# Kernel optimization log

Measured on AMD Instinct MI355X. Metric: run time of the kernel, lower is better.

Reference implementation:

```python
import jax, jax.numpy as jnp
import numpy as np

B, C, H, W = 4, 64, 64, 64  # in_dim hardcoded to 64 by the module's views


def _conv1x1(x, w, b):
    # x: [B,C,H,W], w: [O,C], b: [O]
    return jnp.einsum('bchw,oc->bohw', x, w) + b[None, :, None, None]


def _branch(x, wq, bq, wk, bk, wv, bv):
    b_, c_, h_, w_ = x.shape
    n = h_ * w_
    q = _conv1x1(x, wq, bq).reshape(b_, c_, n)
    k = _conv1x1(x, wk, bk).reshape(b_, c_, n)
    v = _conv1x1(x, wv, bv).reshape(b_, c_, n)
    # scores[b,i,j] = sum_c q[b,c,i] * k[b,c,j]  (no scale factor, as in source)
    s = jax.nn.softmax(jnp.einsum('bci,bcj->bij', q, k), axis=-1)  # [B,N,N]
    # out[b,c,j] = sum_i v[b,c,i] * s[b,i,j]
    return jnp.einsum('bci,bij->bcj', v, s).reshape(b_, c_, h_, w_)


def setup_inputs() -> dict:
    key = jax.random.key(0)
    ks = jax.random.split(key, 17)
    sc = 1.0 / np.sqrt(C)
    d = {'x': jax.random.normal(ks[0], (B, C, H, W), jnp.float32)}
    names = ['qh', 'kh', 'vh', 'ql', 'kl', 'vl']
    for i, nm in enumerate(names):
        d['W_' + nm] = jax.random.normal(ks[1 + 2 * i], (C, C), jnp.float32) * sc
        d['b_' + nm] = jax.random.normal(ks[2 + 2 * i], (C,), jnp.float32) * 0.01
    d['g1'] = jax.random.normal(ks[13], (1,), jnp.float32) * 0.5
    d['g2'] = jax.random.normal(ks[14], (1,), jnp.float32) * 0.5
    d['W_f'] = jax.random.normal(ks[15], (C, 2 * C), jnp.float32) * (1.0 / np.sqrt(2 * C))
    d['b_f'] = jax.random.normal(ks[16], (C,), jnp.float32) * 0.01
    return d


def reference(x, W_qh, b_qh, W_kh, b_kh, W_vh, b_vh, W_ql, b_ql, W_kl, b_kl, W_vl, b_vl, g1, g2, W_f, b_f):
    xh1 = g1[0] * _branch(x, W_qh, b_qh, W_kh, b_kh, W_vh, b_vh)
    xl1 = g2[0] * _branch(x, W_ql, b_ql, W_kl, b_kl, W_vl, b_vl)
    cat = jnp.concatenate([xh1, xl1], axis=1)  # [B,2C,H,W]
    return _conv1x1(cat, W_f, b_f)
```

## Files before the change

kernel.cpp:

```cpp
#include <hip/hip_runtime.h>

#define NN 4096
#define CD 64

typedef __attribute__((ext_vector_type(8))) short bf16x8;
typedef __attribute__((ext_vector_type(4))) float f32x4;

__device__ unsigned short g_Qh[2][4][NN][CD];
__device__ unsigned short g_Ql[2][4][NN][CD];
__device__ unsigned short g_Kh[2][4][NN][CD];
__device__ unsigned short g_Kl[2][4][NN][CD];
__device__ float          g_Vf[2][4][CD][NN];
__device__ unsigned short g_Vh[2][4][CD][NN];
__device__ unsigned short g_Vl[2][4][CD][NN];
__device__ float          g_Op[4][2][4][CD][NN];
__device__ float          g_Zp[4][2][4][NN];

__device__ inline f32x4 mfma16(bf16x8 a, bf16x8 b, f32x4 c) {
  return __builtin_amdgcn_mfma_f32_16x16x32_bf16(a, b, c, 0, 0, 0);
}

__device__ inline void split_bf(float x, unsigned short& h, unsigned short& l) {
  unsigned u = __builtin_bit_cast(unsigned, x);
  h = (unsigned short)(u >> 16);
  float hf = __builtin_bit_cast(float, u & 0xffff0000u);
  unsigned v = __builtin_bit_cast(unsigned, x - hf);
  v += 0x7fffu + ((v >> 16) & 1u);
  l = (unsigned short)(v >> 16);
}

__device__ inline void lds_barrier() {
  asm volatile("s_waitcnt lgkmcnt(0)\n\ts_barrier" ::: "memory");
}

struct ProjArgs {
  const float* x;
  const float* W[6];
  const float* bias[6];
};

__global__ __launch_bounds__(256) void proj_kernel(ProjArgs a) {
  __shared__ float Wt[64][68];
  __shared__ float bs[64];
  const int tid = threadIdx.x;
  const int m = blockIdx.z;
  const float* __restrict__ W = a.W[m];
#pragma unroll
  for (int k = 0; k < 16; ++k) {
    int t = k * 256 + tid;
    Wt[t & 63][t >> 6] = W[t];
  }
  if (tid < 64) bs[tid] = a.bias[m][tid];
  __syncthreads();

  const int b = blockIdx.y;
  const int n = (blockIdx.x << 6) + (tid & 63);
  const int og = tid >> 6;
  const float* __restrict__ xp = a.x + ((size_t)b * CD) * NN + n;

  float acc[16];
#pragma unroll
  for (int k = 0; k < 16; ++k) acc[k] = bs[og * 16 + k];

#pragma unroll 4
  for (int c = 0; c < 64; ++c) {
    float xv = xp[(size_t)c * NN];
    float w[16];
    *(float4*)&w[0]  = *(const float4*)&Wt[c][og * 16 + 0];
    *(float4*)&w[4]  = *(const float4*)&Wt[c][og * 16 + 4];
    *(float4*)&w[8]  = *(const float4*)&Wt[c][og * 16 + 8];
    *(float4*)&w[12] = *(const float4*)&Wt[c][og * 16 + 12];
#pragma unroll
    for (int k = 0; k < 16; ++k) acc[k] += w[k] * xv;
  }

  const int br = m / 3, kind = m % 3;
  if (kind == 2) {
    float* dst = &g_Vf[br][b][0][0] + n;
#pragma unroll
    for (int k = 0; k < 16; ++k) dst[(size_t)(og * 16 + k) * NN] = acc[k];
  } else {
    unsigned short hi[16], lo[16];
#pragma unroll
    for (int k = 0; k < 16; ++k) split_bf(acc[k], hi[k], lo[k]);
    unsigned short* dh = (kind == 0) ? &g_Qh[br][b][n][og * 16] : &g_Kh[br][b][n][og * 16];
    unsigned short* dl = (kind == 0) ? &g_Ql[br][b][n][og * 16] : &g_Kl[br][b][n][og * 16];
    *(uint4*)dh       = *(const uint4*)&hi[0];
    *(uint4*)(dh + 8) = *(const uint4*)&hi[8];
    *(uint4*)dl       = *(const uint4*)&lo[0];
    *(uint4*)(dl + 8) = *(const uint4*)&lo[8];
  }
}

__global__ __launch_bounds__(256) void pass1_kernel() {
  __shared__ float zbuf[2][64];

  const int tid = threadIdx.x;
  const int bid = blockIdx.x;
  const int img = bid & 7;
  const int br = img >> 2, b = img & 3;
  const int js = (bid >> 3) & 3;
  const int i0 = (bid >> 5) << 6;

  const int lane = tid & 63, w = tid >> 6;
  const int wi = w >> 1, wj = w & 1;
  const int lm = lane & 15, q = lane >> 4;

  const unsigned short* __restrict__ QhB = &g_Qh[br][b][0][0];
  const unsigned short* __restrict__ QlB = &g_Ql[br][b][0][0];
  const unsigned short* __restrict__ KhB = &g_Kh[br][b][0][0];
  const unsigned short* __restrict__ KlB = &g_Kl[br][b][0][0];

  bf16x8 qa[2][2][2];
#pragma unroll
  for (int it = 0; it < 2; ++it)
#pragma unroll
    for (int cs = 0; cs < 2; ++cs) {
      size_t off = (size_t)(i0 + wi * 32 + it * 16 + lm) * 64 + cs * 32 + q * 8;
      qa[it][cs][0] = *(const bf16x8*)(QhB + off);
      qa[it][cs][1] = *(const bf16x8*)(QlB + off);
    }

  float zacc[2][4];
#pragma unroll
  for (int it = 0; it < 2; ++it)
#pragma unroll
    for (int r = 0; r < 4; ++r) zacc[it][r] = 0.f;

  const int jwave = wj * 32 + lm;
  for (int tt = 0; tt < 16; ++tt) {
    const int jb = ((js << 4) + tt) << 6;

    bf16x8 kb[2][2][2];
#pragma unroll
    for (int jt = 0; jt < 2; ++jt) {
      size_t rowo = (size_t)(jb + jwave + jt * 16) * 64 + q * 8;
#pragma unroll
      for (int cs = 0; cs < 2; ++cs) {
        kb[jt][cs][0] = *(const bf16x8*)(KhB + rowo + cs * 32);
        kb[jt][cs][1] = *(const bf16x8*)(KlB + rowo + cs * 32);
      }
    }

    const f32x4 zf = {0.f, 0.f, 0.f, 0.f};
#pragma unroll
    for (int it = 0; it < 2; ++it)
#pragma unroll
      for (int jt = 0; jt < 2; ++jt) {
        f32x4 s = mfma16(qa[it][0][0], kb[jt][0][0], zf);
        s = mfma16(qa[it][1][0], kb[jt][1][0], s);
        s = mfma16(qa[it][0][0], kb[jt][0][1], s);
        s = mfma16(qa[it][1][0], kb[jt][1][1], s);
        s = mfma16(qa[it][0][1], kb[jt][0][0], s);
        s = mfma16(qa[it][1][1], kb[jt][1][0], s);
        zacc[it][0] += __expf(s[0]);
        zacc[it][1] += __expf(s[1]);
        zacc[it][2] += __expf(s[2]);
        zacc[it][3] += __expf(s[3]);
      }
  }

#pragma unroll
  for (int mm = 1; mm < 16; mm <<= 1)
#pragma unroll
    for (int it = 0; it < 2; ++it)
#pragma unroll
      for (int r = 0; r < 4; ++r) zacc[it][r] += __shfl_xor(zacc[it][r], mm, 64);

  if (lm == 0) {
#pragma unroll
    for (int it = 0; it < 2; ++it)
#pragma unroll
      for (int r = 0; r < 4; ++r)
        zbuf[wj][wi * 32 + it * 16 + q * 4 + r] = zacc[it][r];
  }
  __syncthreads();
  if (tid < 64) g_Zp[js][br][b][i0 + tid] = zbuf[0][tid] + zbuf[1][tid];
}

__global__ __launch_bounds__(256) void scalev_kernel(const float* __restrict__ g1,
                                                     const float* __restrict__ g2) {
  int idx = blockIdx.x * 256 + threadIdx.x;
  int i4 = idx & 1023;
  int c  = (idx >> 10) & 63;
  int b  = (idx >> 16) & 3;
  int br = idx >> 18;
  float g = br ? g2[0] : g1[0];
  float4 z0 = *(const float4*)&g_Zp[0][br][b][i4 * 4];
  float4 z1 = *(const float4*)&g_Zp[1][br][b][i4 * 4];
  float4 z2 = *(const float4*)&g_Zp[2][br][b][i4 * 4];
  float4 z3 = *(const float4*)&g_Zp[3][br][b][i4 * 4];
  float4 z = {z0.x + z1.x + z2.x + z3.x, z0.y + z1.y + z2.y + z3.y,
              z0.z + z1.z + z2.z + z3.z, z0.w + z1.w + z2.w + z3.w};
  float4 v = *(const float4*)&g_Vf[br][b][c][i4 * 4];
  float vv[4] = {v.x * g / z.x, v.y * g / z.y, v.z * g / z.z, v.w * g / z.w};
  unsigned short h[4], l[4];
#pragma unroll
  for (int r = 0; r < 4; ++r) split_bf(vv[r], h[r], l[r]);
  uint2 uh, ul;
  uh.x = (unsigned)h[0] | ((unsigned)h[1] << 16);
  uh.y = (unsigned)h[2] | ((unsigned)h[3] << 16);
  ul.x = (unsigned)l[0] | ((unsigned)l[1] << 16);
  ul.y = (unsigned)l[2] | ((unsigned)l[3] << 16);
  *(uint2*)&g_Vh[br][b][c][i4 * 4] = uh;
  *(uint2*)&g_Vl[br][b][c][i4 * 4] = ul;
}

__global__ __launch_bounds__(256, 2) void pass2_kernel() {
  __shared__ unsigned short pt_h[64 * 64];
  __shared__ unsigned short pt_l[64 * 64];

  const int tid = threadIdx.x;
  const int bid = blockIdx.x;
  const int img = bid & 7;
  const int br = img >> 2, b = img & 3;
  const int is = (bid >> 3) & 3;
  const int j0 = (bid >> 5) << 6;

  const int lane = tid & 63, w = tid >> 6;
  const int wi = w >> 1, wj = w & 1;
  const int lm = lane & 15, q = lane >> 4;

  const unsigned short* __restrict__ QhB = &g_Qh[br][b][0][0];
  const unsigned short* __restrict__ QlB = &g_Ql[br][b][0][0];
  const unsigned short* __restrict__ KhB = &g_Kh[br][b][0][0];
  const unsigned short* __restrict__ KlB = &g_Kl[br][b][0][0];
  const unsigned short* __restrict__ VhB = &g_Vh[br][b][0][0];
  const unsigned short* __restrict__ VlB = &g_Vl[br][b][0][0];

  bf16x8 kb[2][2][2];
#pragma unroll
  for (int jt = 0; jt < 2; ++jt)
#pragma unroll
    for (int cs = 0; cs < 2; ++cs) {
      size_t off = (size_t)(j0 + wj * 32 + jt * 16 + lm) * 64 + cs * 32 + q * 8;
      kb[jt][cs][0] = *(const bf16x8*)(KhB + off);
      kb[jt][cs][1] = *(const bf16x8*)(KlB + off);
    }

  bf16x8 qa[2][2][2];
  bf16x8 va[2][2][2];
  auto loadQ = [&](int ib) {
#pragma unroll
    for (int it = 0; it < 2; ++it)
#pragma unroll
      for (int cs = 0; cs < 2; ++cs) {
        size_t off = (size_t)(ib + wi * 32 + it * 16 + lm) * 64 + cs * 32 + q * 8;
        qa[it][cs][0] = *(const bf16x8*)(QhB + off);
        qa[it][cs][1] = *(const bf16x8*)(QlB + off);
      }
  };
  auto loadV = [&](int ib) {
#pragma unroll
    for (int ct = 0; ct < 2; ++ct)
#pragma unroll
      for (int ks = 0; ks < 2; ++ks) {
        size_t off = (size_t)(wi * 32 + ct * 16 + lm) * NN + ib + ks * 32 + q * 8;
        va[ct][ks][0] = *(const bf16x8*)(VhB + off);
        va[ct][ks][1] = *(const bf16x8*)(VlB + off);
      }
  };
  const int ibase = is << 10;
  loadQ(ibase);
  loadV(ibase);

  f32x4 oacc[2][2];
#pragma unroll
  for (int ct = 0; ct < 2; ++ct)
#pragma unroll
    for (int jt = 0; jt < 2; ++jt) oacc[ct][jt] = (f32x4){0.f, 0.f, 0.f, 0.f};

  for (int tt = 0; tt < 16; ++tt) {
    const int inext = ibase + ((tt + 1) << 6);
    const f32x4 zf = {0.f, 0.f, 0.f, 0.f};
    f32x4 sacc[2][2];
#pragma unroll
    for (int it = 0; it < 2; ++it)
#pragma unroll
      for (int jt = 0; jt < 2; ++jt) {
        f32x4 s = mfma16(qa[it][0][0], kb[jt][0][0], zf);
        s = mfma16(qa[it][1][0], kb[jt][1][0], s);
        s = mfma16(qa[it][0][0], kb[jt][0][1], s);
        s = mfma16(qa[it][1][0], kb[jt][1][1], s);
        s = mfma16(qa[it][0][1], kb[jt][0][0], s);
        s = mfma16(qa[it][1][1], kb[jt][1][0], s);
        sacc[it][jt] = s;
      }
    if (tt < 15) loadQ(inext);

    uint2 wh[2][2], wl[2][2];
#pragma unroll
    for (int it = 0; it < 2; ++it)
#pragma unroll
      for (int jt = 0; jt < 2; ++jt) {
        unsigned short h[4], l[4];
#pragma unroll
        for (int r = 0; r < 4; ++r) {
          float e = __expf(sacc[it][jt][r]);
          split_bf(e, h[r], l[r]);
        }
        wh[it][jt].x = (unsigned)h[0] | ((unsigned)h[1] << 16);
        wh[it][jt].y = (unsigned)h[2] | ((unsigned)h[3] << 16);
        wl[it][jt].x = (unsigned)l[0] | ((unsigned)l[1] << 16);
        wl[it][jt].y = (unsigned)l[2] | ((unsigned)l[3] << 16);
      }

    lds_barrier();
#pragma unroll
    for (int it = 0; it < 2; ++it)
#pragma unroll
      for (int jt = 0; jt < 2; ++jt) {
        int row = wj * 32 + jt * 16 + lm;
        int byte = row * 128 + (((wi * 64) + it * 32 + q * 8) ^ ((row & 7) << 4));
        *(uint2*)((char*)pt_h + byte) = wh[it][jt];
        *(uint2*)((char*)pt_l + byte) = wl[it][jt];
      }
    lds_barrier();

    bf16x8 pb[2][2][2];
#pragma unroll
    for (int jt = 0; jt < 2; ++jt) {
      int row = wj * 32 + jt * 16 + lm;
      int rb = row * 128, sw = (row & 7) << 4;
#pragma unroll
      for (int ks = 0; ks < 2; ++ks) {
        int byte = rb + ((ks * 64 + q * 16) ^ sw);
        pb[jt][ks][0] = *(const bf16x8*)((const char*)pt_h + byte);
        pb[jt][ks][1] = *(const bf16x8*)((const char*)pt_l + byte);
      }
    }
#pragma unroll
    for (int ct = 0; ct < 2; ++ct)
#pragma unroll
      for (int jt = 0; jt < 2; ++jt) {
        f32x4 o = oacc[ct][jt];
        o = mfma16(va[ct][0][0], pb[jt][0][0], o);
        o = mfma16(va[ct][1][0], pb[jt][1][0], o);
        o = mfma16(va[ct][0][0], pb[jt][0][1], o);
        o = mfma16(va[ct][1][0], pb[jt][1][1], o);
        o = mfma16(va[ct][0][1], pb[jt][0][0], o);
        o = mfma16(va[ct][1][1], pb[jt][1][0], o);
        oacc[ct][jt] = o;
      }
    if (tt < 15) loadV(inext);
  }

  float* __restrict__ Ob = &g_Op[is][br][b][0][0];
#pragma unroll
  for (int ct = 0; ct < 2; ++ct)
#pragma unroll
    for (int jt = 0; jt < 2; ++jt)
#pragma unroll
      for (int r = 0; r < 4; ++r)
        Ob[(size_t)(wi * 32 + ct * 16 + q * 4 + r) * NN + j0 + wj * 32 + jt * 16 + lm] =
            oacc[ct][jt][r];
}

__global__ __launch_bounds__(256) void final_kernel(const float* __restrict__ Wf,
                                                    const float* __restrict__ bf,
                                                    float* __restrict__ out) {
  __shared__ float Wt[128][68];
  __shared__ float bs[64];
  const int tid = threadIdx.x;
#pragma unroll
  for (int k = 0; k < 32; ++k) {
    int t = k * 256 + tid;
    Wt[t & 127][t >> 7] = Wf[t];
  }
  if (tid < 64) bs[tid] = bf[tid];
  __syncthreads();

  const int b = blockIdx.y;
  const int n = (blockIdx.x << 6) + (tid & 63);
  const int og = tid >> 6;
  const size_t PS = (size_t)2 * 4 * CD * NN;

  float acc[16];
#pragma unroll
  for (int k = 0; k < 16; ++k) acc[k] = bs[og * 16 + k];

#pragma unroll
  for (int br = 0; br < 2; ++br) {
    const float* __restrict__ Ob = &g_Op[0][br][b][0][0];
#pragma unroll 4
    for (int c = 0; c < 64; ++c) {
      const float* p = Ob + (size_t)c * NN + n;
      float xv = p[0] + p[PS] + p[2 * PS] + p[3 * PS];
      float wv[16];
      *(float4*)&wv[0]  = *(const float4*)&Wt[br * 64 + c][og * 16 + 0];
      *(float4*)&wv[4]  = *(const float4*)&Wt[br * 64 + c][og * 16 + 4];
      *(float4*)&wv[8]  = *(const float4*)&Wt[br * 64 + c][og * 16 + 8];
      *(float4*)&wv[12] = *(const float4*)&Wt[br * 64 + c][og * 16 + 12];
#pragma unroll
      for (int k = 0; k < 16; ++k) acc[k] += wv[k] * xv;
    }
  }

  float* op = out + ((size_t)b * CD) * NN + n;
#pragma unroll
  for (int k = 0; k < 16; ++k) op[(size_t)(og * 16 + k) * NN] = acc[k];
}

extern "C" void kernel_launch(void* const* d_in, const int* in_sizes, int n_in,
                              void* d_out, int out_size, void* d_ws, size_t ws_size,
                              hipStream_t stream) {
  (void)in_sizes; (void)n_in; (void)d_ws; (void)ws_size; (void)out_size;

  ProjArgs pa;
  pa.x = (const float*)d_in[0];
  for (int m = 0; m < 6; ++m) {
    pa.W[m]    = (const float*)d_in[1 + 2 * m];
    pa.bias[m] = (const float*)d_in[2 + 2 * m];
  }
  const float* g1 = (const float*)d_in[13];
  const float* g2 = (const float*)d_in[14];
  const float* Wf = (const float*)d_in[15];
  const float* bf = (const float*)d_in[16];
  float* out = (float*)d_out;

  proj_kernel<<<dim3(64, 4, 6), 256, 0, stream>>>(pa);
  pass1_kernel<<<dim3(2048), 256, 0, stream>>>();
  scalev_kernel<<<dim3(2048), 256, 0, stream>>>(g1, g2);
  pass2_kernel<<<dim3(2048), 256, 0, stream>>>();
  final_kernel<<<dim3(64, 4), 256, 0, stream>>>(Wf, bf, out);
}
```

Before: 487.5 us.

## Drop low bf16 parts of P and V, restructure pass2 per-wave columns

The second attention pass now uses a single bf16 for the probabilities and the scaled V instead of hi/lo split pairs, which cuts the MFMA count in the PV product by a factor of three and halves V traffic. pass2 is reorganised so each wave owns 16 output columns and loops over all 64 i-tiles, which removes the cross-wave LDS barriers and the 4-way partial-output reduction in final_kernel. pass1 gains K register double-buffering, and both passes raise wave priority with s_setprio around the MFMA blocks. The risks are lower accuracy from single-bf16 P and V, and fewer, longer blocks (512), which may reduce parallelism.

```diff
diff --git a/kernel.cpp b/kernel.cpp
--- a/kernel.cpp
+++ b/kernel.cpp
@@ -11,9 +11,8 @@
 __device__ unsigned short g_Kh[2][4][NN][CD];
 __device__ unsigned short g_Kl[2][4][NN][CD];
 __device__ float          g_Vf[2][4][CD][NN];
-__device__ unsigned short g_Vh[2][4][CD][NN];
-__device__ unsigned short g_Vl[2][4][CD][NN];
-__device__ float          g_Op[4][2][4][CD][NN];
+__device__ unsigned short g_Vb[2][4][CD][NN];
+__device__ float          g_O [2][4][CD][NN];
 __device__ float          g_Zp[4][2][4][NN];
 
 __device__ inline f32x4 mfma16(bf16x8 a, bf16x8 b, f32x4 c) {
@@ -29,8 +28,12 @@
   l = (unsigned short)(v >> 16);
 }
 
-__device__ inline void lds_barrier() {
-  asm volatile("s_waitcnt lgkmcnt(0)\n\ts_barrier" ::: "memory");
+__device__ inline unsigned rne2(float a, float b) {
+  unsigned ua = __builtin_bit_cast(unsigned, a);
+  unsigned ub = __builtin_bit_cast(unsigned, b);
+  ua += 0x7fffu + ((ua >> 16) & 1u);
+  ub += 0x7fffu + ((ub >> 16) & 1u);
+  return (ua >> 16) | (ub & 0xffff0000u);
 }
 
 struct ProjArgs {
@@ -128,36 +131,56 @@
     for (int r = 0; r < 4; ++r) zacc[it][r] = 0.f;
 
   const int jwave = wj * 32 + lm;
-  for (int tt = 0; tt < 16; ++tt) {
+
+  auto loadk = [&](bf16x8 (&dst)[2][2][2], int tt) {
     const int jb = ((js << 4) + tt) << 6;
-
-    bf16x8 kb[2][2][2];
 #pragma unroll
     for (int jt = 0; jt < 2; ++jt) {
       size_t rowo = (size_t)(jb + jwave + jt * 16) * 64 + q * 8;
 #pragma unroll
       for (int cs = 0; cs < 2; ++cs) {
-        kb[jt][cs][0] = *(const bf16x8*)(KhB + rowo + cs * 32);
-        kb[jt][cs][1] = *(const bf16x8*)(KlB + rowo + cs * 32);
+        dst[jt][cs][0] = *(const bf16x8*)(KhB + rowo + cs * 32);
+        dst[jt][cs][1] = *(const bf16x8*)(KlB + rowo + cs * 32);
       }
     }
-
+  };
+
+  auto scomp = [&](bf16x8 (&kb)[2][2][2]) {
     const f32x4 zf = {0.f, 0.f, 0.f, 0.f};
+    f32x4 s[2][2];
+    __builtin_amdgcn_s_setprio(1);
 #pragma unroll
     for (int it = 0; it < 2; ++it)
 #pragma unroll
       for (int jt = 0; jt < 2; ++jt) {
-        f32x4 s = mfma16(qa[it][0][0], kb[jt][0][0], zf);
-        s = mfma16(qa[it][1][0], kb[jt][1][0], s);
-        s = mfma16(qa[it][0][0], kb[jt][0][1], s);
-        s = mfma16(qa[it][1][0], kb[jt][1][1], s);
-        s = mfma16(qa[it][0][1], kb[jt][0][0], s);
-        s = mfma16(qa[it][1][1], kb[jt][1][0], s);
-        zacc[it][0] += __expf(s[0]);
-        zacc[it][1] += __expf(s[1]);
-        zacc[it][2] += __expf(s[2]);
-        zacc[it][3] += __expf(s[3]);
+        f32x4 t = mfma16(qa[it][0][0], kb[jt][0][0], zf);
+        t = mfma16(qa[it][1][0], kb[jt][1][0], t);
+        t = mfma16(qa[it][0][0], kb[jt][0][1], t);
+        t = mfma16(qa[it][1][0], kb[jt][1][1], t);
+        t = mfma16(qa[it][0][1], kb[jt][0][0], t);
+        t = mfma16(qa[it][1][1], kb[jt][1][0], t);
+        s[it][jt] = t;
       }
+    __builtin_amdgcn_s_setprio(0);
+#pragma unroll
+    for (int it = 0; it < 2; ++it)
+#pragma unroll
+      for (int jt = 0; jt < 2; ++jt) {
+        zacc[it][0] += __expf(s[it][jt][0]);
+        zacc[it][1] += __expf(s[it][jt][1]);
+        zacc[it][2] += __expf(s[it][jt][2]);
+        zacc[it][3] += __expf(s[it][jt][3]);
+      }
+  };
+
+  bf16x8 kA[2][2][2], kB[2][2][2];
+  loadk(kA, 0);
+  for (int t2 = 0; t2 < 8; ++t2) {
+    const int to = t2 * 2 + 1;
+    loadk(kB, to);
+    scomp(kA);
+    if (to < 15) loadk(kA, to + 1);
+    scomp(kB);
   }
 
 #pragma unroll
@@ -193,167 +216,115 @@
   float4 z = {z0.x + z1.x + z2.x + z3.x, z0.y + z1.y + z2.y + z3.y,
               z0.z + z1.z + z2.z + z3.z, z0.w + z1.w + z2.w + z3.w};
   float4 v = *(const float4*)&g_Vf[br][b][c][i4 * 4];
-  float vv[4] = {v.x * g / z.x, v.y * g / z.y, v.z * g / z.z, v.w * g / z.w};
-  unsigned short h[4], l[4];
-#pragma unroll
-  for (int r = 0; r < 4; ++r) split_bf(vv[r], h[r], l[r]);
-  uint2 uh, ul;
-  uh.x = (unsigned)h[0] | ((unsigned)h[1] << 16);
-  uh.y = (unsigned)h[2] | ((unsigned)h[3] << 16);
-  ul.x = (unsigned)l[0] | ((unsigned)l[1] << 16);
-  ul.y = (unsigned)l[2] | ((unsigned)l[3] << 16);
-  *(uint2*)&g_Vh[br][b][c][i4 * 4] = uh;
-  *(uint2*)&g_Vl[br][b][c][i4 * 4] = ul;
+  uint2 uh;
+  uh.x = rne2(v.x * g / z.x, v.y * g / z.y);
+  uh.y = rne2(v.z * g / z.z, v.w * g / z.w);
+  *(uint2*)&g_Vb[br][b][c][i4 * 4] = uh;
 }
 
 __global__ __launch_bounds__(256, 2) void pass2_kernel() {
-  __shared__ unsigned short pt_h[64 * 64];
-  __shared__ unsigned short pt_l[64 * 64];
+  __shared__ unsigned short pt[64 * 64];
 
   const int tid = threadIdx.x;
   const int bid = blockIdx.x;
   const int img = bid & 7;
   const int br = img >> 2, b = img & 3;
-  const int is = (bid >> 3) & 3;
-  const int j0 = (bid >> 5) << 6;
+  const int j0 = (bid >> 3) << 6;
 
   const int lane = tid & 63, w = tid >> 6;
-  const int wi = w >> 1, wj = w & 1;
   const int lm = lane & 15, q = lane >> 4;
+  const int row = w * 16 + lm;
+  const int jcol = j0 + row;
+  const int sw = (row & 7) << 4;
 
   const unsigned short* __restrict__ QhB = &g_Qh[br][b][0][0];
   const unsigned short* __restrict__ QlB = &g_Ql[br][b][0][0];
   const unsigned short* __restrict__ KhB = &g_Kh[br][b][0][0];
   const unsigned short* __restrict__ KlB = &g_Kl[br][b][0][0];
-  const unsigned short* __restrict__ VhB = &g_Vh[br][b][0][0];
-  const unsigned short* __restrict__ VlB = &g_Vl[br][b][0][0];
-
-  bf16x8 kb[2][2][2];
-#pragma unroll
-  for (int jt = 0; jt < 2; ++jt)
-#pragma unroll
-    for (int cs = 0; cs < 2; ++cs) {
-      size_t off = (size_t)(j0 + wj * 32 + jt * 16 + lm) * 64 + cs * 32 + q * 8;
-      kb[jt][cs][0] = *(const bf16x8*)(KhB + off);
-      kb[jt][cs][1] = *(const bf16x8*)(KlB + off);
-    }
-
-  bf16x8 qa[2][2][2];
-  bf16x8 va[2][2][2];
+  const unsigned short* __restrict__ VbB = &g_Vb[br][b][0][0];
+
+  bf16x8 kb[2][2];
+#pragma unroll
+  for (int cs = 0; cs < 2; ++cs) {
+    size_t off = (size_t)jcol * 64 + cs * 32 + q * 8;
+    kb[cs][0] = *(const bf16x8*)(KhB + off);
+    kb[cs][1] = *(const bf16x8*)(KlB + off);
+  }
+
+  bf16x8 qa[4][2][2];
+  bf16x8 va[4][2];
   auto loadQ = [&](int ib) {
 #pragma unroll
-    for (int it = 0; it < 2; ++it)
+    for (int it = 0; it < 4; ++it)
 #pragma unroll
       for (int cs = 0; cs < 2; ++cs) {
-        size_t off = (size_t)(ib + wi * 32 + it * 16 + lm) * 64 + cs * 32 + q * 8;
+        size_t off = (size_t)(ib + it * 16 + lm) * 64 + cs * 32 + q * 8;
         qa[it][cs][0] = *(const bf16x8*)(QhB + off);
         qa[it][cs][1] = *(const bf16x8*)(QlB + off);
       }
   };
   auto loadV = [&](int ib) {
 #pragma unroll
-    for (int ct = 0; ct < 2; ++ct)
-#pragma unroll
-      for (int ks = 0; ks < 2; ++ks) {
-        size_t off = (size_t)(wi * 32 + ct * 16 + lm) * NN + ib + ks * 32 + q * 8;
-        va[ct][ks][0] = *(const bf16x8*)(VhB + off);
-        va[ct][ks][1] = *(const bf16x8*)(VlB + off);
-      }
+    for (int ct = 0; ct < 4; ++ct)
+#pragma unroll
+      for (int ks = 0; ks < 2; ++ks)
+        va[ct][ks] = *(const bf16x8*)(VbB + (size_t)(ct * 16 + lm) * NN + ib + ks * 32 + q * 8);
   };
-  const int ibase = is << 10;
-  loadQ(ibase);
-  loadV(ibase);
-
-  f32x4 oacc[2][2];
-#pragma unroll
-  for (int ct = 0; ct < 2; ++ct)
-#pragma unroll
-    for (int jt = 0; jt < 2; ++jt) oacc[ct][jt] = (f32x4){0.f, 0.f, 0.f, 0.f};
-
-  for (int tt = 0; tt < 16; ++tt) {
-    const int inext = ibase + ((tt + 1) << 6);
+  loadQ(0);
+  loadV(0);
+
+  f32x4 oacc[4];
+#pragma unroll
+  for (int ct = 0; ct < 4; ++ct) oacc[ct] = (f32x4){0.f, 0.f, 0.f, 0.f};
+
+  for (int tt = 0; tt < 64; ++tt) {
+    const int inext = (tt + 1) << 6;
     const f32x4 zf = {0.f, 0.f, 0.f, 0.f};
-    f32x4 sacc[2][2];
-#pragma unroll
-    for (int it = 0; it < 2; ++it)
-#pragma unroll
-      for (int jt = 0; jt < 2; ++jt) {
-        f32x4 s = mfma16(qa[it][0][0], kb[jt][0][0], zf);
-        s = mfma16(qa[it][1][0], kb[jt][1][0], s);
-        s = mfma16(qa[it][0][0], kb[jt][0][1], s);
-        s = mfma16(qa[it][1][0], kb[jt][1][1], s);
-        s = mfma16(qa[it][0][1], kb[jt][0][0], s);
-        s = mfma16(qa[it][1][1], kb[jt][1][0], s);
-        sacc[it][jt] = s;
-      }
-    if (tt < 15) loadQ(inext);
-
-    uint2 wh[2][2], wl[2][2];
-#pragma unroll
-    for (int it = 0; it < 2; ++it)
-#pragma unroll
-      for (int jt = 0; jt < 2; ++jt) {
-        unsigned short h[4], l[4];
-#pragma unroll
-        for (int r = 0; r < 4; ++r) {
-          float e = __expf(sacc[it][jt][r]);
-          split_bf(e, h[r], l[r]);
-        }
-        wh[it][jt].x = (unsigned)h[0] | ((unsigned)h[1] << 16);
-        wh[it][jt].y = (unsigned)h[2] | ((unsigned)h[3] << 16);
-        wl[it][jt].x = (unsigned)l[0] | ((unsigned)l[1] << 16);
-        wl[it][jt].y = (unsigned)l[2] | ((unsigned)l[3] << 16);
-      }
-
-    lds_barrier();
-#pragma unroll
-    for (int it = 0; it < 2; ++it)
-#pragma unroll
-      for (int jt = 0; jt < 2; ++jt) {
-        int row = wj * 32 + jt * 16 + lm;
-        int byte = row * 128 + (((wi * 64) + it * 32 + q * 8) ^ ((row & 7) << 4));
-        *(uint2*)((char*)pt_h + byte) = wh[it][jt];
-        *(uint2*)((char*)pt_l + byte) = wl[it][jt];
-      }
-    lds_barrier();
-
-    bf16x8 pb[2][2][2];
-#pragma unroll
-    for (int jt = 0; jt < 2; ++jt) {
-      int row = wj * 32 + jt * 16 + lm;
-      int rb = row * 128, sw = (row & 7) << 4;
-#pragma unroll
-      for (int ks = 0; ks < 2; ++ks) {
-        int byte = rb + ((ks * 64 + q * 16) ^ sw);
-        pb[jt][ks][0] = *(const bf16x8*)((const char*)pt_h + byte);
-        pb[jt][ks][1] = *(const bf16x8*)((const char*)pt_l + byte);
-      }
-    }
-#pragma unroll
-    for (int ct = 0; ct < 2; ++ct)
-#pragma unroll
-      for (int jt = 0; jt < 2; ++jt) {
-        f32x4 o = oacc[ct][jt];
-        o = mfma16(va[ct][0][0], pb[jt][0][0], o);
-        o = mfma16(va[ct][1][0], pb[jt][1][0], o);
-        o = mfma16(va[ct][0][0], pb[jt][0][1], o);
-        o = mfma16(va[ct][1][0], pb[jt][1][1], o);
-        o = mfma16(va[ct][0][1], pb[jt][0][0], o);
-        o = mfma16(va[ct][1][1], pb[jt][1][0], o);
-        oacc[ct][jt] = o;
-      }
-    if (tt < 15) loadV(inext);
-  }
-
-  float* __restrict__ Ob = &g_Op[is][br][b][0][0];
-#pragma unroll
-  for (int ct = 0; ct < 2; ++ct)
-#pragma unroll
-    for (int jt = 0; jt < 2; ++jt)
-#pragma unroll
-      for (int r = 0; r < 4; ++r)
-        Ob[(size_t)(wi * 32 + ct * 16 + q * 4 + r) * NN + j0 + wj * 32 + jt * 16 + lm] =
-            oacc[ct][jt][r];
+    f32x4 sacc[4];
+    __builtin_amdgcn_s_setprio(1);
+#pragma unroll
+    for (int it = 0; it < 4; ++it) {
+      f32x4 s = mfma16(qa[it][0][0], kb[0][0], zf);
+      s = mfma16(qa[it][1][0], kb[1][0], s);
+      s = mfma16(qa[it][0][0], kb[0][1], s);
+      s = mfma16(qa[it][1][0], kb[1][1], s);
+      s = mfma16(qa[it][0][1], kb[0][0], s);
+      s = mfma16(qa[it][1][1], kb[1][0], s);
+      sacc[it] = s;
+    }
+    __builtin_amdgcn_s_setprio(0);
+    if (tt < 63) loadQ(inext);
+
+#pragma unroll
+    for (int it = 0; it < 4; ++it) {
+      uint2 wpk;
+      wpk.x = rne2(__expf(sacc[it][0]), __expf(sacc[it][1]));
+      wpk.y = rne2(__expf(sacc[it][2]), __expf(sacc[it][3]));
+      *(uint2*)((char*)pt + row * 128 + ((it * 32 + q * 8) ^ sw)) = wpk;
+    }
+    asm volatile("s_waitcnt lgkmcnt(0)" ::: "memory");
+    __builtin_amdgcn_sched_barrier(0);
+
+    bf16x8 pb[2];
+#pragma unroll
+    for (int ks = 0; ks < 2; ++ks)
+      pb[ks] = *(const bf16x8*)((const char*)pt + row * 128 + ((ks * 64 + q * 16) ^ sw));
+    __builtin_amdgcn_s_setprio(1);
+#pragma unroll
+    for (int ct = 0; ct < 4; ++ct) {
+      f32x4 o = mfma16(va[ct][0], pb[0], oacc[ct]);
+      oacc[ct] = mfma16(va[ct][1], pb[1], o);
+    }
+    __builtin_amdgcn_s_setprio(0);
+    if (tt < 63) loadV(inext);
+  }
+
+  float* __restrict__ Ob = &g_O[br][b][0][0];
+#pragma unroll
+  for (int ct = 0; ct < 4; ++ct)
+#pragma unroll
+    for (int r = 0; r < 4; ++r)
+      Ob[(size_t)(ct * 16 + q * 4 + r) * NN + jcol] = oacc[ct][r];
 }
 
 __global__ __launch_bounds__(256) void final_kernel(const float* __restrict__ Wf,
@@ -373,7 +344,6 @@
   const int b = blockIdx.y;
   const int n = (blockIdx.x << 6) + (tid & 63);
   const int og = tid >> 6;
-  const size_t PS = (size_t)2 * 4 * CD * NN;
 
   float acc[16];
 #pragma unroll
@@ -381,11 +351,10 @@
 
 #pragma unroll
   for (int br = 0; br < 2; ++br) {
-    const float* __restrict__ Ob = &g_Op[0][br][b][0][0];
+    const float* __restrict__ Ob = &g_O[br][b][0][0];
 #pragma unroll 4
     for (int c = 0; c < 64; ++c) {
-      const float* p = Ob + (size_t)c * NN + n;
-      float xv = p[0] + p[PS] + p[2 * PS] + p[3 * PS];
+      float xv = Ob[(size_t)c * NN + n];
       float wv[16];
       *(float4*)&wv[0]  = *(const float4*)&Wt[br * 64 + c][og * 16 + 0];
       *(float4*)&wv[4]  = *(const float4*)&Wt[br * 64 + c][og * 16 + 4];
@@ -421,6 +390,6 @@
   proj_kernel<<<dim3(64, 4, 6), 256, 0, stream>>>(pa);
   pass1_kernel<<<dim3(2048), 256, 0, stream>>>();
   scalev_kernel<<<dim3(2048), 256, 0, stream>>>(g1, g2);
-  pass2_kernel<<<dim3(2048), 256, 0, stream>>>();
+  pass2_kernel<<<dim3(512), 256, 0, stream>>>();
   final_kernel<<<dim3(64, 4), 256, 0, stream>>>(Wf, bf, out);
 }
```

Measured after the change: 581.3 us. 19.2% more time.
